# Optimization experiments

Measured on AMD Instinct MI355X. Metric: run time of the kernel, lower is better.

Reference implementation:

```python
import jax, jax.numpy as jnp
import numpy as np

N_NODES = 100000
N_EDGES = 6400000
D_FEAT = 128
HIDDEN = 16


def _gcn_conv(x, row, col, W, b, n):
    # PyG GCNConv: add self-loops, symmetric norm, message from row -> aggregated at col
    h = x @ W  # [N, out]
    loop = jnp.arange(n, dtype=row.dtype)
    r = jnp.concatenate([row, loop])
    c = jnp.concatenate([col, loop])
    ones = jnp.ones(r.shape[0], dtype=x.dtype)
    deg = jax.ops.segment_sum(ones, c, num_segments=n)  # in-degree incl. self-loop
    dinv = jnp.where(deg > 0, jax.lax.rsqrt(deg), 0.0)
    norm = dinv[r] * dinv[c]  # [E+N]
    msg = h[r] * norm[:, None]  # [E+N, out]
    out = jax.ops.segment_sum(msg, c, num_segments=n)
    return out + b


def setup_inputs() -> dict:
    key = jax.random.key(0)
    ks = jax.random.split(key, 8)
    x = jax.random.normal(ks[0], (N_NODES, D_FEAT), dtype=jnp.float32)
    edge_attr = jax.random.normal(ks[1], (N_EDGES, 1), dtype=jnp.float32)
    edge_row = jnp.sort(jax.random.randint(ks[2], (N_EDGES,), 0, N_NODES, dtype=jnp.int32)).astype(jnp.int64)
    edge_col = jax.random.randint(ks[3], (N_EDGES,), 0, N_NODES, dtype=jnp.int32).astype(jnp.int64)
    W1 = jax.random.normal(ks[4], (D_FEAT + 1, HIDDEN), dtype=jnp.float32) * (1.0 / np.sqrt(D_FEAT + 1))
    b1 = jnp.zeros((HIDDEN,), dtype=jnp.float32)
    W2 = jax.random.normal(ks[5], (HIDDEN, 1), dtype=jnp.float32) * (1.0 / np.sqrt(HIDDEN))
    b2 = jnp.zeros((1,), dtype=jnp.float32)
    return {"x": x, "edge_attr": edge_attr, "edge_row": edge_row, "edge_col": edge_col,
            "W1": W1, "b1": b1, "W2": W2, "b2": b2}


def reference(x, edge_attr, edge_row, edge_col, W1, b1, W2, b2):
    n = x.shape[0]
    # the original Python loop == segment-sum of edge_attr by source node (rows are sorted)
    x_edge = jax.ops.segment_sum(edge_attr, edge_row, num_segments=n)  # [N, 1]
    h = jnp.concatenate([x, x_edge], axis=1)  # [N, D+1]
    h = _gcn_conv(h, edge_row, edge_col, W1, b1, n)
    h = jax.nn.relu(h)
    # dropout is identity in eval mode
    out = _gcn_conv(h, edge_row, edge_col, W2, b2, n)  # [N, 1]
    return out
```

## Files before the change

### kernel.cpp

```cpp
#include <hip/hip_runtime.h>


#define D_FEAT 128
#define HIDDEN 16
#define TILE 4096
#define CAP 17408u

__device__ inline float bf2f(unsigned short u) {
    union { unsigned x; float f; } t; t.x = ((unsigned)u) << 16; return t.f;
}

__global__ __launch_bounds__(256) void k_init(float* xe, unsigned* gcur, int n, int nb) {
    int t = blockIdx.x * 256 + threadIdx.x;
    if (t < n) xe[t] = 0.f;
    if (t < nb) gcur[t * 16] = (unsigned)t * CAP;
}

__global__ __launch_bounds__(512) void k_sortplace(const int* __restrict__ row,
                                                   const int* __restrict__ col,
                                                   const float* __restrict__ ea,
                                                   float* __restrict__ xe,
                                                   unsigned* __restrict__ gcur,
                                                   unsigned* __restrict__ ebufP,
                                                   int ne, int nb) {
    __shared__ unsigned stage[TILE];
    __shared__ unsigned short sbuck[TILE];
    __shared__ unsigned h[512], base_[512], cursor[512], gb_[512];
    __shared__ unsigned wsum[8];
    int tid = threadIdx.x;
    int lane = tid & 63;
    int w = tid >> 6;
    int tile0 = blockIdx.x * TILE;
    int cnt_t = min(TILE, ne - tile0);
    h[tid] = 0u;
    __syncthreads();
    int rr[8], cc[8];
    float aa[8];
    #pragma unroll
    for (int k = 0; k < 8; ++k) {
        int e = tile0 + tid + k * 512;
        if (e < ne) {
            rr[k] = row[e]; cc[k] = col[e]; aa[k] = ea[e];
            atomicAdd(&h[cc[k] >> 8], 1u);
        } else { rr[k] = -1; cc[k] = 0; aa[k] = 0.f; }
    }
    #pragma unroll
    for (int k = 0; k < 8; ++k) {
        int r = rr[k];
        float a = aa[k];
        #pragma unroll
        for (int d = 1; d < 64; d <<= 1) {
            float up = __shfl_up(a, d);
            int  rup = __shfl_up(r, d);
            if (lane >= d && rup == r) a += up;
        }
        int rdn = __shfl_down(r, 1);
        bool tail = (lane == 63) || (rdn != r);
        if (r >= 0 && tail) unsafeAtomicAdd(&xe[r], a);
    }
    __syncthreads();
    unsigned hv = h[tid];
    unsigned s = hv;
    #pragma unroll
    for (int d = 1; d < 64; d <<= 1) {
        unsigned u = __shfl_up(s, d);
        if (lane >= d) s += u;
    }
    if (lane == 63) wsum[w] = s;
    __syncthreads();
    unsigned woff = 0;
    #pragma unroll
    for (int i = 0; i < 8; ++i) woff += (i < w) ? wsum[i] : 0u;
    unsigned ex = s + woff - hv;
    base_[tid] = ex;
    cursor[tid] = ex;
    if (tid < nb && hv) gb_[tid] = atomicAdd(&gcur[tid * 16], hv);
    __syncthreads();
    #pragma unroll
    for (int k = 0; k < 8; ++k) {
        if (rr[k] >= 0) {
            int b = cc[k] >> 8;
            unsigned p = atomicAdd(&cursor[b], 1u);
            stage[p] = (((unsigned)(cc[k] & 255)) << 24) | (unsigned)rr[k];
            sbuck[p] = (unsigned short)b;
        }
    }
    __syncthreads();
    for (int t = tid; t < cnt_t; t += 512) {
        unsigned b = sbuck[t];
        unsigned pos = gb_[b] + ((unsigned)t - base_[b]);
        if (pos < (b + 1u) * CAP) ebufP[pos] = stage[t];
    }
}

__global__ __launch_bounds__(512) void k_deghist(const unsigned* __restrict__ gcur,
                                                 const unsigned* __restrict__ ebufP,
                                                 unsigned* __restrict__ deg, int n) {
    __shared__ unsigned dg[256];
    int tid = threadIdx.x, b = blockIdx.x;
    if (tid < 256) dg[tid] = 0u;
    __syncthreads();
    unsigned base = (unsigned)b * CAP;
    unsigned m = min(gcur[b * 16] - base, CAP);
    unsigned i = tid;
    for (; i + 1536 < m; i += 2048) {
        unsigned pk0 = ebufP[base + i];
        unsigned pk1 = ebufP[base + i + 512];
        unsigned pk2 = ebufP[base + i + 1024];
        unsigned pk3 = ebufP[base + i + 1536];
        atomicAdd(&dg[pk0 >> 24], 1u);
        atomicAdd(&dg[pk1 >> 24], 1u);
        atomicAdd(&dg[pk2 >> 24], 1u);
        atomicAdd(&dg[pk3 >> 24], 1u);
    }
    for (; i < m; i += 512) atomicAdd(&dg[ebufP[base + i] >> 24], 1u);
    __syncthreads();
    if (tid < 256) {
        int v = b * 256 + tid;
        if (v < n) deg[v] = dg[tid];
    }
}

__global__ __launch_bounds__(256) void k_gemm1(const float* __restrict__ x,
                                               const float* __restrict__ xe,
                                               const unsigned* __restrict__ deg,
                                               const float* __restrict__ W1,
                                               float* __restrict__ g,
                                               unsigned short* __restrict__ gb, int n) {
    __shared__ float WsT[16 * 132];
    __shared__ float xs[64 * 132];
    int tid = threadIdx.x;
    for (int idx = tid; idx < 129 * 16; idx += 256) {
        int k = idx >> 4, j = idx & 15;
        WsT[j * 132 + k] = W1[idx];
    }
    int n0 = blockIdx.x * 64;
    const float4* x4 = (const float4*)x;
    for (int idx = tid; idx < 64 * 32; idx += 256) {
        int r = idx >> 5, c = idx & 31;
        float4 v = (n0 + r < n) ? x4[(size_t)(n0 + r) * 32 + c]
                                : make_float4(0.f, 0.f, 0.f, 0.f);
        *(float4*)&xs[r * 132 + c * 4] = v;
    }
    if (tid < 64) {
        int r = tid;
        xs[r * 132 + 128] = (n0 + r < n) ? xe[n0 + r] : 0.f;
    }
    __syncthreads();
    int j  = tid & 15;
    int nb = tid >> 4;
    const float* wrow = &WsT[j * 132];
    for (int rep = 0; rep < 4; ++rep) {
        int nl = nb + (rep << 4);
        int node = n0 + nl;
        const float* xrow = &xs[nl * 132];
        float acc = 0.f;
        #pragma unroll
        for (int k = 0; k < 128; k += 4) {
            float4 xv = *(const float4*)&xrow[k];
            float4 wv = *(const float4*)&wrow[k];
            acc += xv.x * wv.x;
            acc += xv.y * wv.y;
            acc += xv.z * wv.z;
            acc += xv.w * wv.w;
        }
        acc += xrow[128] * wrow[128];
        if (node < n) {
            float v = acc * rsqrtf((float)deg[node] + 1.0f);
            g[(size_t)node * 16 + j] = v;
            union { float f; unsigned u; } cv; cv.f = v;
            unsigned r16 = (cv.u + 0x7FFFu + ((cv.u >> 16) & 1u)) >> 16;
            gb[(size_t)node * 16 + j] = (unsigned short)r16;
        }
    }
}

__global__ __launch_bounds__(512) void k_agg1s(const unsigned* __restrict__ gcur,
                                               const unsigned* __restrict__ ebufP,
                                               const unsigned* __restrict__ deg,
                                               const unsigned* __restrict__ gu,
                                               const float* __restrict__ g,
                                               const float* __restrict__ b1,
                                               const float* __restrict__ W2,
                                               float* __restrict__ g2, int n) {
    __shared__ unsigned sorted[CAP];
    __shared__ unsigned dg[256], st[256], cur[256];
    __shared__ unsigned wsum[4];
    int tid = threadIdx.x, b = blockIdx.x, lane = tid & 63;
    unsigned base = (unsigned)b * CAP;
    unsigned m = min(gcur[b * 16] - base, CAP);
    unsigned dval = 0, s = 0;
    if (tid < 256) {
        int v = b * 256 + tid;
        dval = (v < n) ? deg[v] : 0u;
        dg[tid] = dval;
        s = dval;
        #pragma unroll
        for (int d = 1; d < 64; d <<= 1) {
            unsigned uu = __shfl_up(s, d);
            if (lane >= d) s += uu;
        }
        if (lane == 63) wsum[tid >> 6] = s;
    }
    __syncthreads();
    if (tid < 256) {
        int w = tid >> 6;
        unsigned woff = 0;
        #pragma unroll
        for (int i = 0; i < 4; ++i) woff += (i < w) ? wsum[i] : 0u;
        unsigned ex = s + woff - dval;
        st[tid] = ex;
        cur[tid] = ex;
    }
    __syncthreads();
    unsigned i = tid;
    for (; i + 1536 < m; i += 2048) {
        unsigned pk0 = ebufP[base + i];
        unsigned pk1 = ebufP[base + i + 512];
        unsigned pk2 = ebufP[base + i + 1024];
        unsigned pk3 = ebufP[base + i + 1536];
        unsigned p0 = atomicAdd(&cur[pk0 >> 24], 1u);
        unsigned p1 = atomicAdd(&cur[pk1 >> 24], 1u);
        unsigned p2 = atomicAdd(&cur[pk2 >> 24], 1u);
        unsigned p3 = atomicAdd(&cur[pk3 >> 24], 1u);
        if (p0 < CAP) sorted[p0] = pk0 & 0xFFFFFFu;
        if (p1 < CAP) sorted[p1] = pk1 & 0xFFFFFFu;
        if (p2 < CAP) sorted[p2] = pk2 & 0xFFFFFFu;
        if (p3 < CAP) sorted[p3] = pk3 & 0xFFFFFFu;
    }
    for (; i < m; i += 512) {
        unsigned pk = ebufP[base + i];
        unsigned p = atomicAdd(&cur[pk >> 24], 1u);
        if (p < CAP) sorted[p] = pk & 0xFFFFFFu;
    }
    __syncthreads();
    const uint2* gu2 = (const uint2*)gu;
    int grp = tid >> 4;
    int u = tid & 3;
    int quarter = (tid >> 2) & 3;
    float4 bb = ((const float4*)b1)[u];
    float4 ww = ((const float4*)W2)[u];
    for (int it = 0; it < 8; ++it) {
        int c = it * 32 + grp;
        int v = b * 256 + c;
        if (v >= n) break;
        unsigned s0 = st[c], e0 = s0 + dg[c];
        float a0 = 0.f, a1 = 0.f, a2 = 0.f, a3 = 0.f;
        float c0 = 0.f, c1 = 0.f, c2 = 0.f, c3 = 0.f;
        unsigned q = s0 + quarter;
        for (; q + 4 < e0; q += 8) {
            unsigned r0 = sorted[q], r1 = sorted[q + 4];
            uint2 w0 = gu2[(size_t)r0 * 4 + u];
            uint2 w1 = gu2[(size_t)r1 * 4 + u];
            a0 += bf2f((unsigned short)w0.x); a1 += bf2f((unsigned short)(w0.x >> 16));
            a2 += bf2f((unsigned short)w0.y); a3 += bf2f((unsigned short)(w0.y >> 16));
            c0 += bf2f((unsigned short)w1.x); c1 += bf2f((unsigned short)(w1.x >> 16));
            c2 += bf2f((unsigned short)w1.y); c3 += bf2f((unsigned short)(w1.y >> 16));
        }
        for (; q < e0; q += 4) {
            uint2 w0 = gu2[(size_t)sorted[q] * 4 + u];
            a0 += bf2f((unsigned short)w0.x); a1 += bf2f((unsigned short)(w0.x >> 16));
            a2 += bf2f((unsigned short)w0.y); a3 += bf2f((unsigned short)(w0.y >> 16));
        }
        a0 += c0; a1 += c1; a2 += c2; a3 += c3;
        a0 += __shfl_xor(a0, 4, 16); a0 += __shfl_xor(a0, 8, 16);
        a1 += __shfl_xor(a1, 4, 16); a1 += __shfl_xor(a1, 8, 16);
        a2 += __shfl_xor(a2, 4, 16); a2 += __shfl_xor(a2, 8, 16);
        a3 += __shfl_xor(a3, 4, 16); a3 += __shfl_xor(a3, 8, 16);
        float di = rsqrtf((float)dg[c] + 1.0f);
        float4 gs = ((const float4*)g)[(size_t)v * 4 + u];
        float v0 = fmaxf(di * (gs.x + a0) + bb.x, 0.f);
        float v1 = fmaxf(di * (gs.y + a1) + bb.y, 0.f);
        float v2 = fmaxf(di * (gs.z + a2) + bb.z, 0.f);
        float v3 = fmaxf(di * (gs.w + a3) + bb.w, 0.f);
        float prd = v0 * ww.x + v1 * ww.y + v2 * ww.z + v3 * ww.w;
        prd += __shfl_down(prd, 2, 4);
        prd += __shfl_down(prd, 1, 4);
        if ((tid & 15) == 0) g2[v] = prd * di;
    }
}

__global__ __launch_bounds__(512) void k_agg2s(const unsigned* __restrict__ gcur,
                                               const unsigned* __restrict__ ebufP,
                                               const unsigned* __restrict__ deg,
                                               const float* __restrict__ g2,
                                               const float* __restrict__ b2,
                                               float* __restrict__ out, int n) {
    __shared__ unsigned sorted[CAP];
    __shared__ unsigned dg[256], st[256], cur[256];
    __shared__ unsigned wsum[4];
    int tid = threadIdx.x, b = blockIdx.x, lane = tid & 63;
    unsigned base = (unsigned)b * CAP;
    unsigned m = min(gcur[b * 16] - base, CAP);
    unsigned dval = 0, s = 0;
    if (tid < 256) {
        int v = b * 256 + tid;
        dval = (v < n) ? deg[v] : 0u;
        dg[tid] = dval;
        s = dval;
        #pragma unroll
        for (int d = 1; d < 64; d <<= 1) {
            unsigned uu = __shfl_up(s, d);
            if (lane >= d) s += uu;
        }
        if (lane == 63) wsum[tid >> 6] = s;
    }
    __syncthreads();
    if (tid < 256) {
        int w = tid >> 6;
        unsigned woff = 0;
        #pragma unroll
        for (int i = 0; i < 4; ++i) woff += (i < w) ? wsum[i] : 0u;
        unsigned ex = s + woff - dval;
        st[tid] = ex;
        cur[tid] = ex;
    }
    __syncthreads();
    unsigned i = tid;
    for (; i + 1536 < m; i += 2048) {
        unsigned pk0 = ebufP[base + i];
        unsigned pk1 = ebufP[base + i + 512];
        unsigned pk2 = ebufP[base + i + 1024];
        unsigned pk3 = ebufP[base + i + 1536];
        unsigned p0 = atomicAdd(&cur[pk0 >> 24], 1u);
        unsigned p1 = atomicAdd(&cur[pk1 >> 24], 1u);
        unsigned p2 = atomicAdd(&cur[pk2 >> 24], 1u);
        unsigned p3 = atomicAdd(&cur[pk3 >> 24], 1u);
        if (p0 < CAP) sorted[p0] = pk0 & 0xFFFFFFu;
        if (p1 < CAP) sorted[p1] = pk1 & 0xFFFFFFu;
        if (p2 < CAP) sorted[p2] = pk2 & 0xFFFFFFu;
        if (p3 < CAP) sorted[p3] = pk3 & 0xFFFFFFu;
    }
    for (; i < m; i += 512) {
        unsigned pk = ebufP[base + i];
        unsigned p = atomicAdd(&cur[pk >> 24], 1u);
        if (p < CAP) sorted[p] = pk & 0xFFFFFFu;
    }
    __syncthreads();
    int c = tid >> 1, half = tid & 1;
    int v = b * 256 + c;
    float a = 0.f;
    unsigned s0 = st[c], e0 = s0 + dg[c];
    unsigned q = s0 + half;
    for (; q + 2 < e0; q += 4) {
        a += g2[sorted[q]];
        a += g2[sorted[q + 2]];
    }
    if (q < e0) a += g2[sorted[q]];
    a += __shfl_xor(a, 1, 2);
    if (half == 0 && v < n) {
        float di = rsqrtf((float)dg[c] + 1.0f);
        out[v] = di * (g2[v] + a) + b2[0];
    }
}

extern "C" void kernel_launch(void* const* d_in, const int* in_sizes, int n_in,
                              void* d_out, int out_size, void* d_ws, size_t ws_size,
                              hipStream_t stream) {
    const float* x   = (const float*)d_in[0];
    const float* ea  = (const float*)d_in[1];
    const int*   row = (const int*)d_in[2];
    const int*   col = (const int*)d_in[3];
    const float* W1  = (const float*)d_in[4];
    const float* b1  = (const float*)d_in[5];
    const float* W2  = (const float*)d_in[6];
    const float* b2  = (const float*)d_in[7];
    float* out = (float*)d_out;

    int n  = in_sizes[0] / D_FEAT;
    int ne = in_sizes[2];
    int nb = (n + 255) >> 8;

    float* ws   = (float*)d_ws;
    float* xe   = ws;
    float* g    = ws + (size_t)n;
    float* g2   = ws + (size_t)17 * n;
    unsigned short* gbuf = (unsigned short*)(ws + (size_t)18 * n);
    unsigned* deg  = (unsigned*)(ws + (size_t)26 * n);
    unsigned* gcur = deg + (size_t)n;
    unsigned* ebufP = gcur + (size_t)nb * 16;

    dim3 blk(256);
    int g_node = (n + 255) / 256;
    int g_tile = (ne + TILE - 1) / TILE;
    int g_gemm = (n + 63) / 64;

    k_init<<<g_node, blk, 0, stream>>>(xe, gcur, n, nb);
    k_sortplace<<<g_tile, 512, 0, stream>>>(row, col, ea, xe, gcur, ebufP, ne, nb);
    k_deghist<<<nb, 512, 0, stream>>>(gcur, ebufP, deg, n);
    k_gemm1<<<g_gemm, blk, 0, stream>>>(x, xe, deg, W1, g, gbuf, n);
    k_agg1s<<<nb, 512, 0, stream>>>(gcur, ebufP, deg, (const unsigned*)gbuf, g, b1, W2, g2, n);
    k_agg2s<<<nb, 512, 0, stream>>>(gcur, ebufP, deg, g2, b2, out, n);
}
```

Baseline: 293.6 us.

## Enlarge sort tiles, precompute bucket offsets, widen agg1 gathers to 16-byte loads

Three separate changes. The sort/place kernel now runs 1024 threads per block over 8192-edge tiles, which halves the number of global bucket-cursor atomics per edge. The degree-histogram kernel now also computes the per-node exclusive prefix and stores it, so both aggregation kernels skip their own block scan and one barrier. The first aggregation gathers 8 bf16 features per lane with uint4 loads instead of 4 with uint2, putting 8 lanes on each node's neighbour list instead of 4. This adds register pressure and a larger shared-memory footprint in the sort kernel, which may lower occupancy.

```diff
diff --git a/kernel.cpp b/kernel.cpp
--- a/kernel.cpp
+++ b/kernel.cpp
@@ -3,7 +3,7 @@
 
 #define D_FEAT 128
 #define HIDDEN 16
-#define TILE 4096
+#define TILE 8192
 #define CAP 17408u
 
 __device__ inline float bf2f(unsigned short u) {
@@ -16,13 +16,13 @@
     if (t < nb) gcur[t * 16] = (unsigned)t * CAP;
 }
 
-__global__ __launch_bounds__(512) void k_sortplace(const int* __restrict__ row,
-                                                   const int* __restrict__ col,
-                                                   const float* __restrict__ ea,
-                                                   float* __restrict__ xe,
-                                                   unsigned* __restrict__ gcur,
-                                                   unsigned* __restrict__ ebufP,
-                                                   int ne, int nb) {
+__global__ __launch_bounds__(1024) void k_sortplace(const int* __restrict__ row,
+                                                    const int* __restrict__ col,
+                                                    const float* __restrict__ ea,
+                                                    float* __restrict__ xe,
+                                                    unsigned* __restrict__ gcur,
+                                                    unsigned* __restrict__ ebufP,
+                                                    int ne, int nb) {
     __shared__ unsigned stage[TILE];
     __shared__ unsigned short sbuck[TILE];
     __shared__ unsigned h[512], base_[512], cursor[512], gb_[512];
@@ -32,13 +32,13 @@
     int w = tid >> 6;
     int tile0 = blockIdx.x * TILE;
     int cnt_t = min(TILE, ne - tile0);
-    h[tid] = 0u;
+    if (tid < 512) h[tid] = 0u;
     __syncthreads();
     int rr[8], cc[8];
     float aa[8];
     #pragma unroll
     for (int k = 0; k < 8; ++k) {
-        int e = tile0 + tid + k * 512;
+        int e = tile0 + tid + k * 1024;
         if (e < ne) {
             rr[k] = row[e]; cc[k] = col[e]; aa[k] = ea[e];
             atomicAdd(&h[cc[k] >> 8], 1u);
@@ -59,22 +59,27 @@
         if (r >= 0 && tail) unsafeAtomicAdd(&xe[r], a);
     }
     __syncthreads();
-    unsigned hv = h[tid];
-    unsigned s = hv;
-    #pragma unroll
-    for (int d = 1; d < 64; d <<= 1) {
-        unsigned u = __shfl_up(s, d);
-        if (lane >= d) s += u;
-    }
-    if (lane == 63) wsum[w] = s;
-    __syncthreads();
-    unsigned woff = 0;
-    #pragma unroll
-    for (int i = 0; i < 8; ++i) woff += (i < w) ? wsum[i] : 0u;
-    unsigned ex = s + woff - hv;
-    base_[tid] = ex;
-    cursor[tid] = ex;
-    if (tid < nb && hv) gb_[tid] = atomicAdd(&gcur[tid * 16], hv);
+    unsigned hv = 0, s = 0;
+    if (tid < 512) {
+        hv = h[tid];
+        s = hv;
+        #pragma unroll
+        for (int d = 1; d < 64; d <<= 1) {
+            unsigned u = __shfl_up(s, d);
+            if (lane >= d) s += u;
+        }
+        if (lane == 63) wsum[w] = s;
+    }
+    __syncthreads();
+    if (tid < 512) {
+        unsigned woff = 0;
+        #pragma unroll
+        for (int i = 0; i < 8; ++i) woff += (i < w) ? wsum[i] : 0u;
+        unsigned ex = s + woff - hv;
+        base_[tid] = ex;
+        cursor[tid] = ex;
+        if (tid < nb && hv) gb_[tid] = atomicAdd(&gcur[tid * 16], hv);
+    }
     __syncthreads();
     #pragma unroll
     for (int k = 0; k < 8; ++k) {
@@ -86,7 +91,7 @@
         }
     }
     __syncthreads();
-    for (int t = tid; t < cnt_t; t += 512) {
+    for (int t = tid; t < cnt_t; t += 1024) {
         unsigned b = sbuck[t];
         unsigned pos = gb_[b] + ((unsigned)t - base_[b]);
         if (pos < (b + 1u) * CAP) ebufP[pos] = stage[t];
@@ -95,9 +100,11 @@
 
 __global__ __launch_bounds__(512) void k_deghist(const unsigned* __restrict__ gcur,
                                                  const unsigned* __restrict__ ebufP,
-                                                 unsigned* __restrict__ deg, int n) {
+                                                 unsigned* __restrict__ deg,
+                                                 unsigned* __restrict__ stG, int n) {
     __shared__ unsigned dg[256];
-    int tid = threadIdx.x, b = blockIdx.x;
+    __shared__ unsigned wsum[4];
+    int tid = threadIdx.x, b = blockIdx.x, lane = tid & 63;
     if (tid < 256) dg[tid] = 0u;
     __syncthreads();
     unsigned base = (unsigned)b * CAP;
@@ -115,9 +122,26 @@
     }
     for (; i < m; i += 512) atomicAdd(&dg[ebufP[base + i] >> 24], 1u);
     __syncthreads();
+    unsigned dval = 0, s = 0;
     if (tid < 256) {
+        dval = dg[tid];
+        s = dval;
+        #pragma unroll
+        for (int d = 1; d < 64; d <<= 1) {
+            unsigned uu = __shfl_up(s, d);
+            if (lane >= d) s += uu;
+        }
+        if (lane == 63) wsum[tid >> 6] = s;
+    }
+    __syncthreads();
+    if (tid < 256) {
+        int w = tid >> 6;
+        unsigned woff = 0;
+        #pragma unroll
+        for (int i2 = 0; i2 < 4; ++i2) woff += (i2 < w) ? wsum[i2] : 0u;
+        unsigned ex = s + woff - dval;
         int v = b * 256 + tid;
-        if (v < n) deg[v] = dg[tid];
+        if (v < n) { deg[v] = dval; stG[v] = base + ex; }
     }
 }
 
@@ -178,6 +202,7 @@
 __global__ __launch_bounds__(512) void k_agg1s(const unsigned* __restrict__ gcur,
                                                const unsigned* __restrict__ ebufP,
                                                const unsigned* __restrict__ deg,
+                                               const unsigned* __restrict__ stG,
                                                const unsigned* __restrict__ gu,
                                                const float* __restrict__ g,
                                                const float* __restrict__ b1,
@@ -185,32 +210,16 @@
                                                float* __restrict__ g2, int n) {
     __shared__ unsigned sorted[CAP];
     __shared__ unsigned dg[256], st[256], cur[256];
-    __shared__ unsigned wsum[4];
-    int tid = threadIdx.x, b = blockIdx.x, lane = tid & 63;
+    int tid = threadIdx.x, b = blockIdx.x;
     unsigned base = (unsigned)b * CAP;
     unsigned m = min(gcur[b * 16] - base, CAP);
-    unsigned dval = 0, s = 0;
     if (tid < 256) {
         int v = b * 256 + tid;
-        dval = (v < n) ? deg[v] : 0u;
+        unsigned dval = (v < n) ? deg[v] : 0u;
+        unsigned sv   = (v < n) ? stG[v] - base : 0u;
         dg[tid] = dval;
-        s = dval;
-        #pragma unroll
-        for (int d = 1; d < 64; d <<= 1) {
-            unsigned uu = __shfl_up(s, d);
-            if (lane >= d) s += uu;
-        }
-        if (lane == 63) wsum[tid >> 6] = s;
-    }
-    __syncthreads();
-    if (tid < 256) {
-        int w = tid >> 6;
-        unsigned woff = 0;
-        #pragma unroll
-        for (int i = 0; i < 4; ++i) woff += (i < w) ? wsum[i] : 0u;
-        unsigned ex = s + woff - dval;
-        st[tid] = ex;
-        cur[tid] = ex;
+        st[tid] = sv;
+        cur[tid] = sv;
     }
     __syncthreads();
     unsigned i = tid;
@@ -234,48 +243,70 @@
         if (p < CAP) sorted[p] = pk & 0xFFFFFFu;
     }
     __syncthreads();
-    const uint2* gu2 = (const uint2*)gu;
+    const uint4* gu4 = (const uint4*)gu;
     int grp = tid >> 4;
-    int u = tid & 3;
-    int quarter = (tid >> 2) & 3;
-    float4 bb = ((const float4*)b1)[u];
-    float4 ww = ((const float4*)W2)[u];
+    int u = tid & 1;
+    int oct = (tid >> 1) & 7;
+    float4 bbA = ((const float4*)b1)[2 * u];
+    float4 bbB = ((const float4*)b1)[2 * u + 1];
+    float4 wwA = ((const float4*)W2)[2 * u];
+    float4 wwB = ((const float4*)W2)[2 * u + 1];
     for (int it = 0; it < 8; ++it) {
         int c = it * 32 + grp;
         int v = b * 256 + c;
         if (v >= n) break;
         unsigned s0 = st[c], e0 = s0 + dg[c];
         float a0 = 0.f, a1 = 0.f, a2 = 0.f, a3 = 0.f;
+        float a4 = 0.f, a5 = 0.f, a6 = 0.f, a7 = 0.f;
         float c0 = 0.f, c1 = 0.f, c2 = 0.f, c3 = 0.f;
-        unsigned q = s0 + quarter;
-        for (; q + 4 < e0; q += 8) {
-            unsigned r0 = sorted[q], r1 = sorted[q + 4];
-            uint2 w0 = gu2[(size_t)r0 * 4 + u];
-            uint2 w1 = gu2[(size_t)r1 * 4 + u];
+        float c4 = 0.f, c5 = 0.f, c6 = 0.f, c7 = 0.f;
+        unsigned q = s0 + oct;
+        for (; q + 8 < e0; q += 16) {
+            uint4 w0 = gu4[(size_t)sorted[q] * 2 + u];
+            uint4 w1 = gu4[(size_t)sorted[q + 8] * 2 + u];
             a0 += bf2f((unsigned short)w0.x); a1 += bf2f((unsigned short)(w0.x >> 16));
             a2 += bf2f((unsigned short)w0.y); a3 += bf2f((unsigned short)(w0.y >> 16));
+            a4 += bf2f((unsigned short)w0.z); a5 += bf2f((unsigned short)(w0.z >> 16));
+            a6 += bf2f((unsigned short)w0.w); a7 += bf2f((unsigned short)(w0.w >> 16));
             c0 += bf2f((unsigned short)w1.x); c1 += bf2f((unsigned short)(w1.x >> 16));
             c2 += bf2f((unsigned short)w1.y); c3 += bf2f((unsigned short)(w1.y >> 16));
-        }
-        for (; q < e0; q += 4) {
-            uint2 w0 = gu2[(size_t)sorted[q] * 4 + u];
+            c4 += bf2f((unsigned short)w1.z); c5 += bf2f((unsigned short)(w1.z >> 16));
+            c6 += bf2f((unsigned short)w1.w); c7 += bf2f((unsigned short)(w1.w >> 16));
+        }
+        for (; q < e0; q += 8) {
+            uint4 w0 = gu4[(size_t)sorted[q] * 2 + u];
             a0 += bf2f((unsigned short)w0.x); a1 += bf2f((unsigned short)(w0.x >> 16));
             a2 += bf2f((unsigned short)w0.y); a3 += bf2f((unsigned short)(w0.y >> 16));
+            a4 += bf2f((unsigned short)w0.z); a5 += bf2f((unsigned short)(w0.z >> 16));
+            a6 += bf2f((unsigned short)w0.w); a7 += bf2f((unsigned short)(w0.w >> 16));
         }
         a0 += c0; a1 += c1; a2 += c2; a3 += c3;
-        a0 += __shfl_xor(a0, 4, 16); a0 += __shfl_xor(a0, 8, 16);
-        a1 += __shfl_xor(a1, 4, 16); a1 += __shfl_xor(a1, 8, 16);
-        a2 += __shfl_xor(a2, 4, 16); a2 += __shfl_xor(a2, 8, 16);
-        a3 += __shfl_xor(a3, 4, 16); a3 += __shfl_xor(a3, 8, 16);
+        a4 += c4; a5 += c5; a6 += c6; a7 += c7;
+        #pragma unroll
+        for (int d = 2; d <= 8; d <<= 1) {
+            a0 += __shfl_xor(a0, d, 16);
+            a1 += __shfl_xor(a1, d, 16);
+            a2 += __shfl_xor(a2, d, 16);
+            a3 += __shfl_xor(a3, d, 16);
+            a4 += __shfl_xor(a4, d, 16);
+            a5 += __shfl_xor(a5, d, 16);
+            a6 += __shfl_xor(a6, d, 16);
+            a7 += __shfl_xor(a7, d, 16);
+        }
         float di = rsqrtf((float)dg[c] + 1.0f);
-        float4 gs = ((const float4*)g)[(size_t)v * 4 + u];
-        float v0 = fmaxf(di * (gs.x + a0) + bb.x, 0.f);
-        float v1 = fmaxf(di * (gs.y + a1) + bb.y, 0.f);
-        float v2 = fmaxf(di * (gs.z + a2) + bb.z, 0.f);
-        float v3 = fmaxf(di * (gs.w + a3) + bb.w, 0.f);
-        float prd = v0 * ww.x + v1 * ww.y + v2 * ww.z + v3 * ww.w;
-        prd += __shfl_down(prd, 2, 4);
-        prd += __shfl_down(prd, 1, 4);
+        float4 gA = ((const float4*)g)[(size_t)v * 4 + 2 * u];
+        float4 gB = ((const float4*)g)[(size_t)v * 4 + 2 * u + 1];
+        float v0 = fmaxf(di * (gA.x + a0) + bbA.x, 0.f);
+        float v1 = fmaxf(di * (gA.y + a1) + bbA.y, 0.f);
+        float v2 = fmaxf(di * (gA.z + a2) + bbA.z, 0.f);
+        float v3 = fmaxf(di * (gA.w + a3) + bbA.w, 0.f);
+        float v4 = fmaxf(di * (gB.x + a4) + bbB.x, 0.f);
+        float v5 = fmaxf(di * (gB.y + a5) + bbB.y, 0.f);
+        float v6 = fmaxf(di * (gB.z + a6) + bbB.z, 0.f);
+        float v7 = fmaxf(di * (gB.w + a7) + bbB.w, 0.f);
+        float prd = v0 * wwA.x + v1 * wwA.y + v2 * wwA.z + v3 * wwA.w
+                  + v4 * wwB.x + v5 * wwB.y + v6 * wwB.z + v7 * wwB.w;
+        prd += __shfl_xor(prd, 1, 16);
         if ((tid & 15) == 0) g2[v] = prd * di;
     }
 }
@@ -283,37 +314,22 @@
 __global__ __launch_bounds__(512) void k_agg2s(const unsigned* __restrict__ gcur,
                                                const unsigned* __restrict__ ebufP,
                                                const unsigned* __restrict__ deg,
+                                               const unsigned* __restrict__ stG,
                                                const float* __restrict__ g2,
                                                const float* __restrict__ b2,
                                                float* __restrict__ out, int n) {
     __shared__ unsigned sorted[CAP];
     __shared__ unsigned dg[256], st[256], cur[256];
-    __shared__ unsigned wsum[4];
-    int tid = threadIdx.x, b = blockIdx.x, lane = tid & 63;
+    int tid = threadIdx.x, b = blockIdx.x;
     unsigned base = (unsigned)b * CAP;
     unsigned m = min(gcur[b * 16] - base, CAP);
-    unsigned dval = 0, s = 0;
     if (tid < 256) {
         int v = b * 256 + tid;
-        dval = (v < n) ? deg[v] : 0u;
+        unsigned dval = (v < n) ? deg[v] : 0u;
+        unsigned sv   = (v < n) ? stG[v] - base : 0u;
         dg[tid] = dval;
-        s = dval;
-        #pragma unroll
-        for (int d = 1; d < 64; d <<= 1) {
-            unsigned uu = __shfl_up(s, d);
-            if (lane >= d) s += uu;
-        }
-        if (lane == 63) wsum[tid >> 6] = s;
-    }
-    __syncthreads();
-    if (tid < 256) {
-        int w = tid >> 6;
-        unsigned woff = 0;
-        #pragma unroll
-        for (int i = 0; i < 4; ++i) woff += (i < w) ? wsum[i] : 0u;
-        unsigned ex = s + woff - dval;
-        st[tid] = ex;
-        cur[tid] = ex;
+        st[tid] = sv;
+        cur[tid] = sv;
     }
     __syncthreads();
     unsigned i = tid;
@@ -377,7 +393,8 @@
     float* g2   = ws + (size_t)17 * n;
     unsigned short* gbuf = (unsigned short*)(ws + (size_t)18 * n);
     unsigned* deg  = (unsigned*)(ws + (size_t)26 * n);
-    unsigned* gcur = deg + (size_t)n;
+    unsigned* stG  = deg + (size_t)n;
+    unsigned* gcur = stG + (size_t)n;
     unsigned* ebufP = gcur + (size_t)nb * 16;
 
     dim3 blk(256);
@@ -386,9 +403,9 @@
     int g_gemm = (n + 63) / 64;
 
     k_init<<<g_node, blk, 0, stream>>>(xe, gcur, n, nb);
-    k_sortplace<<<g_tile, 512, 0, stream>>>(row, col, ea, xe, gcur, ebufP, ne, nb);
-    k_deghist<<<nb, 512, 0, stream>>>(gcur, ebufP, deg, n);
+    k_sortplace<<<g_tile, 1024, 0, stream>>>(row, col, ea, xe, gcur, ebufP, ne, nb);
+    k_deghist<<<nb, 512, 0, stream>>>(gcur, ebufP, deg, stG, n);
     k_gemm1<<<g_gemm, blk, 0, stream>>>(x, xe, deg, W1, g, gbuf, n);
-    k_agg1s<<<nb, 512, 0, stream>>>(gcur, ebufP, deg, (const unsigned*)gbuf, g, b1, W2, g2, n);
-    k_agg2s<<<nb, 512, 0, stream>>>(gcur, ebufP, deg, g2, b2, out, n);
-}
+    k_agg1s<<<nb, 512, 0, stream>>>(gcur, ebufP, deg, stG, (const unsigned*)gbuf, g, b1, W2, g2, n);
+    k_agg2s<<<nb, 512, 0, stream>>>(gcur, ebufP, deg, stG, g2, b2, out, n);
+}
```

Measured after the change: 284.2 us. 3.2% less time.
